# Kernel optimization log

Hardware: AMD Instinct MI355X
Metric: run time of the kernel (lower is better)

Reference implementation:

```python
import jax, jax.numpy as jnp
import numpy as np

# ---- config (from Mamba2Config defaults) ----
D_MODEL = 1024
D_STATE = 128
D_CONV = 4
EXPAND = 2
HEADDIM = 64
D_INNER = EXPAND * D_MODEL          # 2048
NHEADS = D_INNER // HEADDIM         # 32
CONV_DIM = D_INNER + 2 * D_STATE    # 2304 (ngroups=1)
D_IN_PROJ = 2 * D_INNER + 2 * D_STATE + NHEADS  # 4384
INTER = ((int(D_MODEL * 8 / 3) + 63) // 64) * 64  # 2752
EPS = 1e-6
BATCH, SEQLEN = 2, 1024


def rmsnorm(x, w):
    return x * jax.lax.rsqrt(jnp.mean(x * x, axis=-1, keepdims=True) + EPS) * w


def setup_inputs() -> dict:
    key = jax.random.key(0)
    ks = jax.random.split(key, 16)
    s = 0.02
    return {
        "hidden_states": jax.random.normal(ks[0], (BATCH, SEQLEN, D_MODEL), jnp.float32),
        "norm_w": jnp.ones((D_MODEL,), jnp.float32),
        "in_proj_w": jax.random.normal(ks[1], (D_IN_PROJ, D_MODEL), jnp.float32) * s,
        "conv_w": jax.random.normal(ks[2], (CONV_DIM, D_CONV), jnp.float32) * 0.2,
        "conv_b": jnp.zeros((CONV_DIM,), jnp.float32),
        "dt_bias": jax.random.normal(ks[3], (NHEADS,), jnp.float32) * 0.5,
        "A_log": jnp.log(jax.random.uniform(ks[4], (NHEADS,), jnp.float32, 1.0, 16.0)),
        "D": jnp.ones((NHEADS,), jnp.float32) + jax.random.normal(ks[5], (NHEADS,), jnp.float32) * 0.05,
        "ssm_norm_w": jnp.ones((D_INNER,), jnp.float32),
        "out_proj_w": jax.random.normal(ks[6], (D_MODEL, D_INNER), jnp.float32) * s,
        "post_norm_w": jnp.ones((D_MODEL,), jnp.float32),
        "gate_w": jax.random.normal(ks[7], (INTER, D_MODEL), jnp.float32) * s,
        "up_w": jax.random.normal(ks[8], (INTER, D_MODEL), jnp.float32) * s,
        "down_w": jax.random.normal(ks[9], (D_MODEL, INTER), jnp.float32) * s,
    }


def _mixer(u, in_proj_w, conv_w, conv_b, dt_bias, A_log, D, ssm_norm_w, out_proj_w):
    b, l, _ = u.shape
    zxbcdt = u @ in_proj_w.T                              # (b,l,4384)
    z = zxbcdt[..., :D_INNER]                             # gate
    xBC = zxbcdt[..., D_INNER:D_INNER + CONV_DIM]
    dt = zxbcdt[..., -NHEADS:]

    # causal depthwise conv1d (kernel D_CONV) + SiLU
    xp = jnp.pad(xBC, ((0, 0), (D_CONV - 1, 0), (0, 0)))
    xBC = sum(xp[:, k:k + l, :] * conv_w[:, k] for k in range(D_CONV)) + conv_b
    xBC = jax.nn.silu(xBC)

    xs = xBC[..., :D_INNER].reshape(b, l, NHEADS, HEADDIM)   # (b,l,h,p)
    Bm = xBC[..., D_INNER:D_INNER + D_STATE]                  # (b,l,n)
    Cm = xBC[..., -D_STATE:]                                  # (b,l,n)

    dt = jax.nn.softplus(dt + dt_bias)                        # (b,l,h)
    A = -jnp.exp(A_log)                                       # (h,)

    def step(h, inp):
        dt_t, x_t, B_t, C_t = inp                             # (b,h),(b,h,p),(b,n),(b,n)
        dA = jnp.exp(dt_t * A)                                # (b,h)
        h = h * dA[..., None, None] + jnp.einsum('bh,bhp,bn->bhpn', dt_t, x_t, B_t)
        y_t = jnp.einsum('bhpn,bn->bhp', h, C_t)
        return h, y_t

    h0 = jnp.zeros((b, NHEADS, HEADDIM, D_STATE), u.dtype)
    xsT = (jnp.moveaxis(dt, 1, 0), jnp.moveaxis(xs, 1, 0),
           jnp.moveaxis(Bm, 1, 0), jnp.moveaxis(Cm, 1, 0))
    _, yT = jax.lax.scan(step, h0, xsT)                       # (l,b,h,p)
    y = jnp.moveaxis(yT, 0, 1) + D[None, None, :, None] * xs  # skip term
    y = y.reshape(b, l, D_INNER)

    # gated RMSNorm (norm_before_gate=False): normalize y*silu(z)
    y = rmsnorm(y * jax.nn.silu(z), ssm_norm_w)
    return y @ out_proj_w.T


def reference(hidden_states, norm_w, in_proj_w, conv_w, conv_b, dt_bias, A_log, D,
              ssm_norm_w, out_proj_w, post_norm_w, gate_w, up_w, down_w):
    res = hidden_states
    h = rmsnorm(hidden_states, norm_w)
    h = _mixer(h, in_proj_w, conv_w, conv_b, dt_bias, A_log, D, ssm_norm_w, out_proj_w)
    x = res + h
    res = x
    h = rmsnorm(x, post_norm_w)
    h = (jax.nn.silu(h @ gate_w.T) * (h @ up_w.T)) @ down_w.T  # SwiGLU MLP
    return res + h
```

## Files before the change

### kernel.cpp

```cpp
#include <hip/hip_runtime.h>
#include <hip/hip_bf16.h>

#define SEQLEN   1024
#define NTOK     2048
#define DMODEL   1024
#define DSTATE   128
#define DINNER   2048
#define NHEADS   32
#define HEADDIM  64
#define CONVDIM  2304
#define DINPROJ  4384
#define INTER    2752
#define Q        64
#define NCHUNK   16

typedef __hip_bfloat16 bf16;
typedef unsigned short ushort_t;
typedef __attribute__((ext_vector_type(8))) short bf16x8;
typedef __attribute__((ext_vector_type(4))) float f32x4;
typedef __attribute__((ext_vector_type(4))) unsigned short u16x4;

__device__ __forceinline__ float bf2f(bf16 x) { return __bfloat162float(x); }
__device__ __forceinline__ float bfu2f(ushort_t u) {
    return __uint_as_float(((unsigned)u) << 16);
}
__device__ __forceinline__ ushort_t f2bfu(float x) {
    union { bf16 h; ushort_t u; } c; c.h = __float2bfloat16(x); return c.u;
}

__device__ __forceinline__ void glds16(const void* g, void* l) {
    __builtin_amdgcn_global_load_lds(
        (const __attribute__((address_space(1))) void*)g,
        (__attribute__((address_space(3))) void*)l, 16, 0, 0);
}

__device__ inline float block_reduce_sum(float v) {
    __shared__ float red[4];
    #pragma unroll
    for (int off = 32; off >= 1; off >>= 1) v += __shfl_down(v, off);
    int lane = threadIdx.x & 63, w = threadIdx.x >> 6;
    if (lane == 0) red[w] = v;
    __syncthreads();
    return red[0] + red[1] + red[2] + red[3];
}

__global__ __launch_bounds__(256) void f2bf_kernel(
    const float* __restrict__ src, ushort_t* __restrict__ dst, int n)
{
    const int i = (blockIdx.x * 256 + threadIdx.x) * 4;
    if (i < n) {
        const f32x4 v = *(const f32x4*)(src + i);
        u16x4 o;
        #pragma unroll
        for (int k = 0; k < 4; k++) o[k] = f2bfu(v[k]);
        *(u16x4*)(dst + i) = o;
    }
}

#define NWOP (DMODEL * DINNER)
#define NWG  (INTER * DMODEL)
__global__ __launch_bounds__(256) void convert_weights_kernel(
    const float* __restrict__ wop, const float* __restrict__ wg,
    const float* __restrict__ wu, const float* __restrict__ wd,
    ushort_t* __restrict__ dWop, ushort_t* __restrict__ dWgu,
    ushort_t* __restrict__ dWdn)
{
    const int i4 = (blockIdx.x * 256 + threadIdx.x) * 4;
    const float* src;
    ushort_t* dst;
    if (i4 < NWOP) { src = wop + i4; dst = dWop + i4; }
    else if (i4 < NWOP + NWG) {
        const int e = i4 - NWOP, row = e >> 10, col = e & 1023;
        src = wg + e; dst = dWgu + ((size_t)(2 * row) << 10) + col;
    } else if (i4 < NWOP + 2 * NWG) {
        const int e = i4 - NWOP - NWG, row = e >> 10, col = e & 1023;
        src = wu + e; dst = dWgu + ((size_t)(2 * row + 1) << 10) + col;
    } else if (i4 < NWOP + 3 * NWG) {
        const int e = i4 - NWOP - 2 * NWG;
        src = wd + e; dst = dWdn + e;
    } else return;
    const f32x4 v = *(const f32x4*)src;
    u16x4 o;
    #pragma unroll
    for (int k = 0; k < 4; k++) o[k] = f2bfu(v[k]);
    *(u16x4*)dst = o;
}

__global__ __launch_bounds__(256) void rmsnorm1024_kernel(
    const float* __restrict__ x, const float* __restrict__ w, bf16* __restrict__ out)
{
    const int token = blockIdx.x, t = threadIdx.x;
    float v[4]; float ss = 0.f;
    #pragma unroll
    for (int i = 0; i < 4; i++) {
        v[i] = x[(size_t)token * DMODEL + t * 4 + i];
        ss += v[i] * v[i];
    }
    ss = block_reduce_sum(ss);
    const float scale = rsqrtf(ss * (1.0f / DMODEL) + 1e-6f);
    #pragma unroll
    for (int i = 0; i < 4; i++)
        out[(size_t)token * DMODEL + t * 4 + i] =
            __float2bfloat16(v[i] * scale * w[t * 4 + i]);
}

template <int EPI, int MT, int NT>
__global__ __launch_bounds__(256) void gemm_bf(
    const bf16* __restrict__ A, const bf16* __restrict__ W,
    float* __restrict__ Cf, const float* __restrict__ resid_f,
    bf16* __restrict__ out_bf, int M, int N, int K)
{
    __shared__ ushort_t As[2][MT * 64];
    __shared__ ushort_t Bs[2][NT * 64];
    const int tid = threadIdx.x;
    const int w = tid >> 6, lane = tid & 63;

    const int gdx = gridDim.x, gdy = gridDim.y;
    const int nwg = gdx * gdy;
    const int orig = blockIdx.x + gdx * blockIdx.y;
    const int q8 = nwg >> 3, r8 = nwg & 7;
    const int xcd = orig & 7, lin = orig >> 3;
    const int wg = (xcd < r8 ? xcd * (q8 + 1) : r8 * (q8 + 1) + (xcd - r8) * q8) + lin;
    const int m0 = (wg % gdy) * MT;
    const int n0 = (wg / gdy) * NT;

    const int srow = tid >> 3;
    const int scol = (((tid & 7) ^ (srow & 7)) * 8);
    const bf16* Agp[MT / 32];
    const bf16* Wgp[NT / 32];
    #pragma unroll
    for (int i = 0; i < MT / 32; i++)
        Agp[i] = A + (size_t)(m0 + i * 32 + srow) * K + scol;
    #pragma unroll
    for (int i = 0; i < NT / 32; i++) {
        const int nr = n0 + i * 32 + srow;
        Wgp[i] = W + (size_t)(nr < N ? nr : 0) * K + scol;
    }

    const int wy = w >> 1, wx = w & 1;
    const int fr = lane & 15;
    const int fq = lane >> 4;
    constexpr int MI = MT / 32;
    constexpr int NJ = NT / 32;
    f32x4 acc[MI][NJ];
    #pragma unroll
    for (int i = 0; i < MI; i++)
        #pragma unroll
        for (int j = 0; j < NJ; j++)
            acc[i][j] = (f32x4){0.f, 0.f, 0.f, 0.f};

    const int nk = K >> 6;

    {
        ushort_t* sa = &As[0][w * 512];
        ushort_t* sb = &Bs[0][w * 512];
        #pragma unroll
        for (int i = 0; i < MT / 32; i++) glds16(Agp[i], sa + i * 2048);
        #pragma unroll
        for (int i = 0; i < NT / 32; i++) glds16(Wgp[i], sb + i * 2048);
    }
    __syncthreads();

    for (int kt = 0; kt < nk; ++kt) {
        const int cur = kt & 1;
        if (kt + 1 < nk) {
            const int koff = (kt + 1) << 6;
            ushort_t* sa = &As[cur ^ 1][w * 512];
            ushort_t* sb = &Bs[cur ^ 1][w * 512];
            #pragma unroll
            for (int i = 0; i < MT / 32; i++) glds16(Agp[i] + koff, sa + i * 2048);
            #pragma unroll
            for (int i = 0; i < NT / 32; i++) glds16(Wgp[i] + koff, sb + i * 2048);
        }
        const ushort_t* ca = As[cur];
        const ushort_t* cb = Bs[cur];
        #pragma unroll
        for (int ks = 0; ks < 2; ks++) {
            bf16x8 af[MI], bfv[NJ];
            #pragma unroll
            for (int i = 0; i < MI; i++) {
                const int r = wy * (MT / 2) + i * 16 + fr;
                const int g = ks * 4 + fq;
                af[i] = *(const bf16x8*)&ca[r * 64 + ((g ^ (r & 7)) * 8)];
            }
            #pragma unroll
            for (int j = 0; j < NJ; j++) {
                const int r = wx * (NT / 2) + j * 16 + fr;
                const int g = ks * 4 + fq;
                bfv[j] = *(const bf16x8*)&cb[r * 64 + ((g ^ (r & 7)) * 8)];
            }
            #pragma unroll
            for (int i = 0; i < MI; i++)
                #pragma unroll
                for (int j = 0; j < NJ; j++)
                    acc[i][j] = __builtin_amdgcn_mfma_f32_16x16x32_bf16(
                        af[i], bfv[j], acc[i][j], 0, 0, 0);
        }
        __syncthreads();
    }

    #pragma unroll
    for (int i = 0; i < MI; i++) {
        #pragma unroll
        for (int j = 0; j < NJ; j++) {
            const int mb = m0 + wy * (MT / 2) + i * 16 + (lane >> 4) * 4;
            const int nn = n0 + wx * (NT / 2) + j * 16 + (lane & 15);
            if (nn < N) {
                #pragma unroll
                for (int r = 0; r < 4; r++) {
                    if (EPI == 2) {
                        const float g = acc[i][j][r];
                        const float u = __shfl_xor(g, 1);
                        if (!(lane & 1)) {
                            const float a = (g / (1.f + expf(-g))) * u;
                            out_bf[(size_t)(mb + r) * (N / 2) + (nn >> 1)] =
                                __float2bfloat16(a);
                        }
                    } else {
                        const size_t idx = (size_t)(mb + r) * N + nn;
                        float v = acc[i][j][r];
                        if (EPI == 1) v += resid_f[idx];
                        Cf[idx] = v;
                    }
                }
            }
        }
    }
}

__global__ __launch_bounds__(256) void conv_silu_kernel(
    const float* __restrict__ zx, const float* __restrict__ cw,
    const float* __restrict__ cb, ushort_t* __restrict__ out)
{
    const int idx = blockIdx.x * 256 + threadIdx.x;
    if (idx >= NTOK * CONVDIM) return;
    const int c = idx % CONVDIM;
    const int token = idx / CONVDIM;
    const int l = token & (SEQLEN - 1);
    float acc = cb[c];
    #pragma unroll
    for (int k = 0; k < 4; k++) {
        const int ls = l - 3 + k;
        if (ls >= 0)
            acc += zx[(size_t)(token - 3 + k) * DINPROJ + DINNER + c] * cw[c * 4 + k];
    }
    out[(size_t)token * CONVDIM + c] = f2bfu(acc / (1.f + expf(-acc)));
}

__global__ __launch_bounds__(256) void dt_softplus_kernel(
    const float* __restrict__ zx, const float* __restrict__ dtb,
    float* __restrict__ out)
{
    const int idx = blockIdx.x * 256 + threadIdx.x;
    const int h = idx & (NHEADS - 1);
    const int token = idx >> 5;
    float v = zx[(size_t)token * DINPROJ + (DINNER + CONVDIM) + h] + dtb[h];
    out[idx] = (v > 20.f) ? v : log1pf(expf(v));
}

__global__ __launch_bounds__(256) void chunk_state_kernel(
    const ushort_t* __restrict__ cvb, const float* __restrict__ dtb,
    const float* __restrict__ A_log, float* __restrict__ ccum,
    ushort_t* __restrict__ Sbuf)
{
    const int bx = blockIdx.x;
    const int bh = bx >> 4, c = bx & 15;
    const int b = bh >> 5, h = bh & 31;
    const int t = threadIdx.x;
    const int w = t >> 6, lane = t & 63;
    const int wy = w >> 1, wx = w & 1;
    const int fr = lane & 15, fk = (lane >> 4) * 8, cr = (lane >> 4) * 4;
    const int tok0 = b * SEQLEN + c * Q;
    const float A = -expf(A_log[h]);

    __shared__ ushort_t sXT[64 * 88];
    __shared__ ushort_t sBT[128 * 88];
    __shared__ float sW[64];

    if (t < 64) {
        const float d = dtb[(size_t)(tok0 + t) * NHEADS + h];
        float s = d;
        #pragma unroll
        for (int off = 1; off < 64; off <<= 1) {
            const float up = __shfl_up(s, off);
            if (t >= off) s += up;
        }
        const float total = __shfl(s, 63);
        sW[t] = expf(A * (total - s)) * d;
        if (t == 63) ccum[bh * NCHUNK + c] = A * total;
    }
    __syncthreads();

    for (int i = t; i < 64 * 64; i += 256) {
        const int l = i >> 6, p = i & 63;
        const float v = bfu2f(cvb[(size_t)(tok0 + l) * CONVDIM + h * HEADDIM + p]);
        sXT[p * 88 + l] = f2bfu(sW[l] * v);
    }
    for (int i = t; i < 128 * 64; i += 256) {
        const int l = i >> 7, n = i & 127;
        sBT[n * 88 + l] = cvb[(size_t)(tok0 + l) * CONVDIM + DINNER + n];
    }
    __syncthreads();

    f32x4 acc[2][4];
    #pragma unroll
    for (int i = 0; i < 2; i++)
        #pragma unroll
        for (int j = 0; j < 4; j++)
            acc[i][j] = (f32x4){0.f, 0.f, 0.f, 0.f};
    #pragma unroll
    for (int k0 = 0; k0 < 64; k0 += 32) {
        bf16x8 af[2], bfv[4];
        #pragma unroll
        for (int i = 0; i < 2; i++)
            af[i] = *(const bf16x8*)&sXT[(wy * 32 + i * 16 + fr) * 88 + fk + k0];
        #pragma unroll
        for (int j = 0; j < 4; j++)
            bfv[j] = *(const bf16x8*)&sBT[(wx * 64 + j * 16 + fr) * 88 + fk + k0];
        #pragma unroll
        for (int i = 0; i < 2; i++)
            #pragma unroll
            for (int j = 0; j < 4; j++)
                acc[i][j] = __builtin_amdgcn_mfma_f32_16x16x32_bf16(
                    af[i], bfv[j], acc[i][j], 0, 0, 0);
    }
    const size_t slot = (size_t)(bh * NCHUNK + c) * 64 * 128;
    #pragma unroll
    for (int i = 0; i < 2; i++) {
        #pragma unroll
        for (int j = 0; j < 4; j++) {
            #pragma unroll
            for (int r = 0; r < 4; r++) {
                const int pr = wy * 32 + i * 16 + cr + r;
                const int nn = wx * 64 + j * 16 + fr;
                Sbuf[slot + pr * 128 + nn] = f2bfu(acc[i][j][r]);
            }
        }
    }
}

__global__ __launch_bounds__(256) void stitch_kernel(
    const float* __restrict__ ccum, ushort_t* __restrict__ Sbuf)
{
    const int bh = blockIdx.x >> 2, ng = blockIdx.x & 3;
    const int t = threadIdx.x, p = t >> 2, q = t & 3;
    float H[8];
    #pragma unroll
    for (int j = 0; j < 8; j++) H[j] = 0.f;
    for (int c = 0; c < NCHUNK; c++) {
        const float P = expf(ccum[bh * NCHUNK + c]);
        const size_t slot = ((size_t)(bh * NCHUNK + c) * 64 + p) * 128 + ng * 32;
        #pragma unroll
        for (int jj = 0; jj < 2; jj++) {
            const u16x4 sv4 = *(const u16x4*)&Sbuf[slot + q * 4 + 16 * jj];
            u16x4 hv4;
            #pragma unroll
            for (int k = 0; k < 4; k++) hv4[k] = f2bfu(H[jj * 4 + k]);
            *(u16x4*)&Sbuf[slot + q * 4 + 16 * jj] = hv4;
            #pragma unroll
            for (int k = 0; k < 4; k++)
                H[jj * 4 + k] = P * H[jj * 4 + k] + bfu2f(sv4[k]);
        }
    }
}

__global__ __launch_bounds__(256) void chunk_scan_mfma_kernel(
    const ushort_t* __restrict__ cvb, const float* __restrict__ dtb,
    const float* __restrict__ A_log, const float* __restrict__ Dh,
    const ushort_t* __restrict__ Sbuf, bf16* __restrict__ ybuf)
{
    const int bx = blockIdx.x;
    const int bh = bx >> 4, c = bx & 15;
    const int b = bh >> 5, h = bh & 31;
    const int t = threadIdx.x;
    const int w = t >> 6, lane = t & 63;
    const int wy = w >> 1, wx = w & 1;
    const int fr = lane & 15;
    const int fk = (lane >> 4) * 8;
    const int cr = (lane >> 4) * 4;
    const int tok0 = b * SEQLEN + c * Q;
    const float A = -expf(A_log[h]);
    const float Dv = Dh[h];

    __shared__ ushort_t sB[64 * 136];
    __shared__ ushort_t sC[64 * 136];
    __shared__ ushort_t sH[64 * 136];
    __shared__ ushort_t sXT[64 * 72];
    __shared__ ushort_t sM[64 * 72];
    __shared__ float    sCum[64];
    __shared__ float    sDtv[64];

    for (int i = t; i < 64 * 32; i += 256) {
        const int row = i >> 5, col = (i & 31) * 4;
        const size_t base = (size_t)(tok0 + row) * CONVDIM;
        *(u16x4*)&sB[row * 136 + col] = *(const u16x4*)&cvb[base + DINNER + col];
        *(u16x4*)&sC[row * 136 + col] = *(const u16x4*)&cvb[base + DINNER + DSTATE + col];
    }
    for (int i = t; i < 64 * 32; i += 256) {
        const int p = i >> 5, l0 = (i & 31) * 2;
        const ushort_t x0 = cvb[(size_t)(tok0 + l0)     * CONVDIM + h * HEADDIM + p];
        const ushort_t x1 = cvb[(size_t)(tok0 + l0 + 1) * CONVDIM + h * HEADDIM + p];
        *(unsigned*)&sXT[p * 72 + l0] = ((unsigned)x1 << 16) | x0;
    }
    {
        const size_t slot = (size_t)(bh * NCHUNK + c) * 64 * 128;
        for (int i = t * 4; i < 64 * 128; i += 1024) {
            const int row = i >> 7, col = i & 127;
            *(u16x4*)&sH[row * 136 + col] = *(const u16x4*)&Sbuf[slot + row * 128 + col];
        }
    }
    if (t < 64) {
        const float d = dtb[(size_t)(tok0 + t) * NHEADS + h];
        float s = d;
        #pragma unroll
        for (int off = 1; off < 64; off <<= 1) {
            const float up = __shfl_up(s, off);
            if (t >= off) s += up;
        }
        sCum[t] = A * s;
        sDtv[t] = d;
    }
    __syncthreads();

    f32x4 accg[2][2];
    #pragma unroll
    for (int i = 0; i < 2; i++)
        #pragma unroll
        for (int j = 0; j < 2; j++)
            accg[i][j] = (f32x4){0.f, 0.f, 0.f, 0.f};
    #pragma unroll
    for (int k0 = 0; k0 < 128; k0 += 32) {
        bf16x8 af[2], bfv[2];
        #pragma unroll
        for (int i = 0; i < 2; i++)
            af[i] = *(const bf16x8*)&sC[(wy * 32 + i * 16 + fr) * 136 + fk + k0];
        #pragma unroll
        for (int j = 0; j < 2; j++)
            bfv[j] = *(const bf16x8*)&sB[(wx * 32 + j * 16 + fr) * 136 + fk + k0];
        #pragma unroll
        for (int i = 0; i < 2; i++)
            #pragma unroll
            for (int j = 0; j < 2; j++)
                accg[i][j] = __builtin_amdgcn_mfma_f32_16x16x32_bf16(
                    af[i], bfv[j], accg[i][j], 0, 0, 0);
    }
    __syncthreads();

    #pragma unroll
    for (int i = 0; i < 2; i++) {
        #pragma unroll
        for (int j = 0; j < 2; j++) {
            #pragma unroll
            for (int r = 0; r < 4; r++) {
                const int l  = wy * 32 + i * 16 + cr + r;
                const int jc = wx * 32 + j * 16 + fr;
                const float v = (jc <= l)
                    ? accg[i][j][r] * expf(sCum[l] - sCum[jc]) * sDtv[jc] : 0.f;
                sM[l * 72 + jc] = f2bfu(v);
            }
        }
    }
    for (int i = t; i < 64 * 32; i += 256) {
        const int row = i >> 5, col = (i & 31) * 4;
        const float sc = expf(sCum[row]);
        u16x4 v = *(const u16x4*)&sC[row * 136 + col];
        #pragma unroll
        for (int k = 0; k < 4; k++) v[k] = f2bfu(bfu2f(v[k]) * sc);
        *(u16x4*)&sC[row * 136 + col] = v;
    }
    __syncthreads();

    f32x4 accy[2][2];
    #pragma unroll
    for (int i = 0; i < 2; i++)
        #pragma unroll
        for (int j = 0; j < 2; j++)
            accy[i][j] = (f32x4){0.f, 0.f, 0.f, 0.f};
    #pragma unroll
    for (int k0 = 0; k0 < 64; k0 += 32) {
        bf16x8 af[2], bfv[2];
        #pragma unroll
        for (int i = 0; i < 2; i++)
            af[i] = *(const bf16x8*)&sM[(wy * 32 + i * 16 + fr) * 72 + fk + k0];
        #pragma unroll
        for (int j = 0; j < 2; j++)
            bfv[j] = *(const bf16x8*)&sXT[(wx * 32 + j * 16 + fr) * 72 + fk + k0];
        #pragma unroll
        for (int i = 0; i < 2; i++)
            #pragma unroll
            for (int j = 0; j < 2; j++)
                accy[i][j] = __builtin_amdgcn_mfma_f32_16x16x32_bf16(
                    af[i], bfv[j], accy[i][j], 0, 0, 0);
    }
    #pragma unroll
    for (int k0 = 0; k0 < 128; k0 += 32) {
        bf16x8 af[2], bfv[2];
        #pragma unroll
        for (int i = 0; i < 2; i++)
            af[i] = *(const bf16x8*)&sC[(wy * 32 + i * 16 + fr) * 136 + fk + k0];
        #pragma unroll
        for (int j = 0; j < 2; j++)
            bfv[j] = *(const bf16x8*)&sH[(wx * 32 + j * 16 + fr) * 136 + fk + k0];
        #pragma unroll
        for (int i = 0; i < 2; i++)
            #pragma unroll
            for (int j = 0; j < 2; j++)
                accy[i][j] = __builtin_amdgcn_mfma_f32_16x16x32_bf16(
                    af[i], bfv[j], accy[i][j], 0, 0, 0);
    }

    #pragma unroll
    for (int i = 0; i < 2; i++) {
        #pragma unroll
        for (int j = 0; j < 2; j++) {
            #pragma unroll
            for (int r = 0; r < 4; r++) {
                const int l = wy * 32 + i * 16 + cr + r;
                const int p = wx * 32 + j * 16 + fr;
                const float x = bfu2f(sXT[p * 72 + l]);
                ybuf[(size_t)(tok0 + l) * DINNER + h * HEADDIM + p] =
                    __float2bfloat16(accy[i][j][r] + Dv * x);
            }
        }
    }
}

__global__ __launch_bounds__(256) void gated_rmsnorm_kernel(
    const bf16* __restrict__ y, const float* __restrict__ zx,
    const float* __restrict__ w, bf16* __restrict__ out)
{
    const int token = blockIdx.x, t = threadIdx.x;
    const bf16* yr = y + (size_t)token * DINNER;
    const float* zr = zx + (size_t)token * DINPROJ;
    float v[8]; float ss = 0.f;
    #pragma unroll
    for (int i = 0; i < 8; i++) {
        const int idx = t * 8 + i;
        const float zz = zr[idx];
        const float val = bf2f(yr[idx]) * (zz / (1.f + expf(-zz)));
        v[i] = val; ss += val * val;
    }
    ss = block_reduce_sum(ss);
    const float scale = rsqrtf(ss * (1.0f / DINNER) + 1e-6f);
    #pragma unroll
    for (int i = 0; i < 8; i++) {
        const int idx = t * 8 + i;
        out[(size_t)token * DINNER + idx] =
            __float2bfloat16(v[i] * scale * w[idx]);
    }
}

extern "C" void kernel_launch(void* const* d_in, const int* in_sizes, int n_in,
                              void* d_out, int out_size, void* d_ws, size_t ws_size,
                              hipStream_t stream) {
    const float* hidden     = (const float*)d_in[0];
    const float* norm_w     = (const float*)d_in[1];
    const float* in_proj_w  = (const float*)d_in[2];
    const float* conv_w     = (const float*)d_in[3];
    const float* conv_b     = (const float*)d_in[4];
    const float* dt_bias    = (const float*)d_in[5];
    const float* A_log      = (const float*)d_in[6];
    const float* Dh         = (const float*)d_in[7];
    const float* ssm_norm_w = (const float*)d_in[8];
    const float* out_proj_w = (const float*)d_in[9];
    const float* post_norm_w= (const float*)d_in[10];
    const float* gate_w     = (const float*)d_in[11];
    const float* up_w       = (const float*)d_in[12];
    const float* down_w     = (const float*)d_in[13];
    float* out = (float*)d_out;

    float* ws = (float*)d_ws;
    bf16*  h_norm = (bf16*)(ws);
    float* zx     = ws + 1048576;
    ushort_t* cvb = (ushort_t*)(ws + 10027008);
    float* dtb    = ws + 14745600;
    float* ccum   = ws + 14811136;
    ushort_t* Sbuf= (ushort_t*)(ws + 14812160);
    float* xbuf   = ws + 19006464;
    bf16*  ybuf   = (bf16*)(ws + 21103616);
    bf16*  ynorm  = (bf16*)(ws + 22152192);
    ushort_t* Wip = (ushort_t*)(ws + 10027008);
    ushort_t* Wop = (ushort_t*)(ws + 1048576);
    ushort_t* Wgu = (ushort_t*)(ws + 2097152);
    ushort_t* Wdn = (ushort_t*)(ws + 4915200);
    bf16*  act    = (bf16*)(ws + 6324224);
    bf16*  h2     = h_norm;

    f2bf_kernel<<<4384, 256, 0, stream>>>(in_proj_w, Wip, DINPROJ * DMODEL);
    rmsnorm1024_kernel<<<NTOK, 256, 0, stream>>>(hidden, norm_w, h_norm);
    gemm_bf<0, 128, 64><<<dim3(69, 16), 256, 0, stream>>>(h_norm, (const bf16*)Wip, zx,
        nullptr, nullptr, NTOK, DINPROJ, DMODEL);
    conv_silu_kernel<<<(NTOK * CONVDIM) / 256, 256, 0, stream>>>(zx, conv_w, conv_b, cvb);
    dt_softplus_kernel<<<(NTOK * NHEADS) / 256, 256, 0, stream>>>(zx, dt_bias, dtb);
    chunk_state_kernel<<<1024, 256, 0, stream>>>(cvb, dtb, A_log, ccum, Sbuf);
    stitch_kernel<<<256, 256, 0, stream>>>(ccum, Sbuf);
    chunk_scan_mfma_kernel<<<1024, 256, 0, stream>>>(cvb, dtb, A_log, Dh, Sbuf, ybuf);
    gated_rmsnorm_kernel<<<NTOK, 256, 0, stream>>>(ybuf, zx, ssm_norm_w, ynorm);
    convert_weights_kernel<<<(NWOP + 3 * NWG) / 1024, 256, 0, stream>>>(
        out_proj_w, gate_w, up_w, down_w, Wop, Wgu, Wdn);
    gemm_bf<1, 64, 64><<<dim3(16, 32), 256, 0, stream>>>(ynorm, (const bf16*)Wop, xbuf,
        hidden, nullptr, NTOK, DMODEL, DINNER);
    rmsnorm1024_kernel<<<NTOK, 256, 0, stream>>>(xbuf, post_norm_w, h2);
    gemm_bf<2, 128, 64><<<dim3(86, 16), 256, 0, stream>>>(h2, (const bf16*)Wgu,
        nullptr, nullptr, act, NTOK, 2 * INTER, DMODEL);
    gemm_bf<1, 64, 64><<<dim3(16, 32), 256, 0, stream>>>(act, (const bf16*)Wdn, out,
        xbuf, nullptr, NTOK, DMODEL, INTER);
}
```

Baseline: 345.7 us.

## Triple-buffer GEMM LDS staging with partial vmcnt waits

The bf16 GEMM moves from a double-buffered LDS pipeline to a three-stage one, issuing global-to-LDS loads two k-tiles ahead. A custom fence waits only until the oldest stage's loads have landed (partial vmcnt) and then barriers, instead of a full __syncthreads drain. The goal is to hide more global load latency behind MFMA work. In exchange LDS use per block grows by half, which can lower occupancy, and correctness depends on the hardcoded vmcnt values matching the number of loads issued per stage.

```diff
diff --git a/kernel.cpp b/kernel.cpp
--- a/kernel.cpp
+++ b/kernel.cpp
@@ -32,6 +32,18 @@
     __builtin_amdgcn_global_load_lds(
         (const __attribute__((address_space(1))) void*)g,
         (__attribute__((address_space(3))) void*)l, 16, 0, 0);
+}
+
+template <int N>
+__device__ __forceinline__ void pipe_fence() {
+    if constexpr (N == 6)
+        asm volatile("s_waitcnt vmcnt(6) lgkmcnt(0)" ::: "memory");
+    else if constexpr (N == 4)
+        asm volatile("s_waitcnt vmcnt(4) lgkmcnt(0)" ::: "memory");
+    else
+        asm volatile("s_waitcnt vmcnt(0) lgkmcnt(0)" ::: "memory");
+    __builtin_amdgcn_s_barrier();
+    __builtin_amdgcn_sched_barrier(0);
 }
 
 __device__ inline float block_reduce_sum(float v) {
@@ -110,10 +122,11 @@
     float* __restrict__ Cf, const float* __restrict__ resid_f,
     bf16* __restrict__ out_bf, int M, int N, int K)
 {
-    __shared__ ushort_t As[2][MT * 64];
-    __shared__ ushort_t Bs[2][NT * 64];
+    __shared__ ushort_t As[3][MT * 64];
+    __shared__ ushort_t Bs[3][NT * 64];
     const int tid = threadIdx.x;
     const int w = tid >> 6, lane = tid & 63;
+    constexpr int NLD = MT / 32 + NT / 32;
 
     const int gdx = gridDim.x, gdy = gridDim.y;
     const int nwg = gdx * gdy;
@@ -151,27 +164,25 @@
 
     const int nk = K >> 6;
 
-    {
-        ushort_t* sa = &As[0][w * 512];
-        ushort_t* sb = &Bs[0][w * 512];
-        #pragma unroll
-        for (int i = 0; i < MT / 32; i++) glds16(Agp[i], sa + i * 2048);
-        #pragma unroll
-        for (int i = 0; i < NT / 32; i++) glds16(Wgp[i], sb + i * 2048);
-    }
-    __syncthreads();
-
+    #define STAGE(buf, koff) do {                                         \
+        ushort_t* sa_ = &As[buf][w * 512];                                \
+        ushort_t* sb_ = &Bs[buf][w * 512];                                \
+        _Pragma("unroll")                                                 \
+        for (int i_ = 0; i_ < MT / 32; i_++)                              \
+            glds16(Agp[i_] + (koff), sa_ + i_ * 2048);                    \
+        _Pragma("unroll")                                                 \
+        for (int i_ = 0; i_ < NT / 32; i_++)                              \
+            glds16(Wgp[i_] + (koff), sb_ + i_ * 2048);                    \
+    } while (0)
+
+    STAGE(0, 0);
+    STAGE(1, 64);
+    pipe_fence<NLD>();
+
+    int cur = 0, stg = 2;
     for (int kt = 0; kt < nk; ++kt) {
-        const int cur = kt & 1;
-        if (kt + 1 < nk) {
-            const int koff = (kt + 1) << 6;
-            ushort_t* sa = &As[cur ^ 1][w * 512];
-            ushort_t* sb = &Bs[cur ^ 1][w * 512];
-            #pragma unroll
-            for (int i = 0; i < MT / 32; i++) glds16(Agp[i] + koff, sa + i * 2048);
-            #pragma unroll
-            for (int i = 0; i < NT / 32; i++) glds16(Wgp[i] + koff, sb + i * 2048);
-        }
+        const bool pf = (kt + 2 < nk);
+        if (pf) STAGE(stg, (kt + 2) << 6);
         const ushort_t* ca = As[cur];
         const ushort_t* cb = Bs[cur];
         #pragma unroll
@@ -196,8 +207,12 @@
                     acc[i][j] = __builtin_amdgcn_mfma_f32_16x16x32_bf16(
                         af[i], bfv[j], acc[i][j], 0, 0, 0);
         }
-        __syncthreads();
-    }
+        if (pf)                    pipe_fence<NLD>();
+        else if (kt + 1 < nk)      pipe_fence<0>();
+        cur = (cur == 2) ? 0 : cur + 1;
+        stg = (stg == 2) ? 0 : stg + 1;
+    }
+    #undef STAGE
 
     #pragma unroll
     for (int i = 0; i < MI; i++) {
```

Result: slower. 375.6 us (+8.7%).
